# Performance work log

Hardware: AMD Instinct MI355X
Metric: run time of the kernel (lower is better)

## Reference

```python
import jax, jax.numpy as jnp
import numpy as np

D = 1024
H = 16
L = 2048
B = 2
EPS = 1e-5


def setup_inputs() -> dict:
    key = jax.random.key(0)
    ks = jax.random.split(key, 12)
    s = 0.02
    return {
        "x": jax.random.normal(ks[0], (B, L, D), dtype=jnp.float32),
        "ln1_w": jnp.ones((D,), jnp.float32),
        "ln1_b": jnp.zeros((D,), jnp.float32),
        "ln2_w": jnp.ones((D,), jnp.float32),
        "ln2_b": jnp.zeros((D,), jnp.float32),
        "attn_w": jax.random.normal(ks[1], (D, 3 * D), jnp.float32) * s,
        "attn_b": jnp.zeros((3 * D,), jnp.float32),
        "proj_w": jax.random.normal(ks[2], (D, D), jnp.float32) * s,
        "proj_b": jnp.zeros((D,), jnp.float32),
        "fc1_w": jax.random.normal(ks[3], (D, 4 * D), jnp.float32) * s,
        "fc1_b": jnp.zeros((4 * D,), jnp.float32),
        "fc2_w": jax.random.normal(ks[4], (4 * D, D), jnp.float32) * s,
        "fc2_b": jnp.zeros((D,), jnp.float32),
    }


def layernorm(x, w, b):
    mu = jnp.mean(x, axis=-1, keepdims=True)
    var = jnp.mean(jnp.square(x - mu), axis=-1, keepdims=True)
    return (x - mu) * jax.lax.rsqrt(var + EPS) * w + b


def reference(x, ln1_w, ln1_b, ln2_w, ln2_b, attn_w, attn_b,
              proj_w, proj_b, fc1_w, fc1_b, fc2_w, fc2_b):
    Bsz, Lq, C = x.shape
    hd = C // H

    # --- attention branch ---
    h = layernorm(x, ln1_w, ln1_b)
    qkv = h @ attn_w + attn_b                      # [B, L, 3C]
    q, k, v = jnp.split(qkv, 3, axis=-1)
    q = q.reshape(Bsz, Lq, H, hd).transpose(0, 2, 1, 3)  # [B, H, L, hd]
    k = k.reshape(Bsz, Lq, H, hd).transpose(0, 2, 1, 3)
    v = v.reshape(Bsz, Lq, H, hd).transpose(0, 2, 1, 3)

    # NOTE: original scales by 1/sqrt(embedding_dim), not sqrt(head_dim)
    att = jnp.einsum('bhqd,bhkd->bhqk', q, k) / jnp.sqrt(jnp.float32(C))
    causal = jnp.tril(jnp.ones((Lq, Lq), dtype=bool))
    att = jnp.where(causal[None, None], att, jnp.float32(-jnp.inf))
    att = jax.nn.softmax(att, axis=-1)
    y = jnp.einsum('bhqk,bhkd->bhqd', att, v)      # [B, H, L, hd]
    y = y.transpose(0, 2, 1, 3).reshape(Bsz, Lq, C)
    y = y @ proj_w + proj_b
    x = x + y

    # --- MLP branch ---
    h = layernorm(x, ln2_w, ln2_b)
    h = jax.nn.gelu(h @ fc1_w + fc1_b, approximate=False)
    h = h @ fc2_w + fc2_b
    return x + h
```

## Files before the change

### kernel.cpp

```cpp
#include <hip/hip_runtime.h>

#define Bsz 2
#define Lq  2048
#define Dm  1024
#define Hh  16

typedef __attribute__((ext_vector_type(8))) short bf16x8;
typedef __attribute__((ext_vector_type(4))) float f32x4;

#define MFMA16(a, b, c) __builtin_amdgcn_mfma_f32_16x16x32_bf16((a), (b), (c), 0, 0, 0)
#define EXP2F(x) __builtin_amdgcn_exp2f(x)

__device__ __forceinline__ short f2bf(float f) {
    union { float f; unsigned u; } v; v.f = f;
    unsigned r = v.u + 0x7fffu + ((v.u >> 16) & 1u);
    return (short)(r >> 16);
}

__device__ __forceinline__ float bf2f(unsigned short s) {
    union { float f; unsigned u; } t; t.u = ((unsigned)s) << 16;
    return t.f;
}

__device__ __forceinline__ int pk2(float a, float b) {
    union { float f; unsigned u; } ua, ub; ua.f = a; ub.f = b;
    return (int)((ua.u >> 16) | (ub.u & 0xffff0000u));
}

__device__ __forceinline__ void gload16(const void* g, void* l) {
    __builtin_amdgcn_global_load_lds((const __attribute__((address_space(1))) void*)g,
                                     (__attribute__((address_space(3))) void*)l,
                                     16, 0, 0);
}

__global__ __launch_bounds__(256) void ln_bf16(const float* __restrict__ x,
                                               const float* __restrict__ w,
                                               const float* __restrict__ b,
                                               short* __restrict__ out) {
    const int row = blockIdx.x;
    const int tid = threadIdx.x;
    const float4 v = ((const float4*)(x + (size_t)row * 1024))[tid];
    float s = v.x + v.y + v.z + v.w;
    float q = v.x * v.x + v.y * v.y + v.z * v.z + v.w * v.w;
    for (int off = 32; off > 0; off >>= 1) {
        s += __shfl_down(s, off);
        q += __shfl_down(q, off);
    }
    __shared__ float red[8];
    const int wave = tid >> 6;
    if ((tid & 63) == 0) { red[wave] = s; red[wave + 4] = q; }
    __syncthreads();
    s = red[0] + red[1] + red[2] + red[3];
    q = red[4] + red[5] + red[6] + red[7];
    const float mu = s * (1.0f / 1024.0f);
    const float var = q * (1.0f / 1024.0f) - mu * mu;
    const float rstd = rsqrtf(var + 1e-5f);
    const float4 wv = ((const float4*)w)[tid];
    const float4 bv = ((const float4*)b)[tid];
    short4 o;
    o.x = f2bf((v.x - mu) * rstd * wv.x + bv.x);
    o.y = f2bf((v.y - mu) * rstd * wv.y + bv.y);
    o.z = f2bf((v.z - mu) * rstd * wv.z + bv.z);
    o.w = f2bf((v.w - mu) * rstd * wv.w + bv.w);
    ((short4*)(out + (size_t)row * 1024))[tid] = o;
}

__global__ __launch_bounds__(256) void tr_cvt_all(
    const float* __restrict__ attnw, const float* __restrict__ projw,
    const float* __restrict__ fc1w,  const float* __restrict__ fc2w,
    short* __restrict__ attnwT, short* __restrict__ projwT,
    short* __restrict__ fc1wT,  short* __restrict__ fc2wT) {
    int id = blockIdx.x;
    const float* W; short* Wt; int K, N, bx, by;
    if (id < 3072)      { W = attnw; Wt = attnwT; K = 1024; N = 3072; bx = id % 96;  by = id / 96; }
    else if (id < 4096) { id -= 3072; W = projw; Wt = projwT; K = 1024; N = 1024; bx = id & 31; by = id >> 5; }
    else if (id < 8192) { id -= 4096; W = fc1w;  Wt = fc1wT;  K = 1024; N = 4096; bx = id & 127; by = id >> 7; }
    else                { id -= 8192; W = fc2w;  Wt = fc2wT;  K = 4096; N = 1024; bx = id & 31; by = id >> 5; }
    __shared__ float t[32][33];
    const int n0 = bx * 32, k0 = by * 32;
    const int tx = threadIdx.x & 31, ty = threadIdx.x >> 5;
#pragma unroll
    for (int i = 0; i < 4; i++)
        t[ty + i * 8][tx] = W[(size_t)(k0 + ty + i * 8) * N + n0 + tx];
    __syncthreads();
#pragma unroll
    for (int i = 0; i < 4; i++)
        Wt[(size_t)(n0 + ty + i * 8) * K + k0 + tx] = f2bf(t[tx][ty + i * 8]);
}

template <int EP>
__global__ __launch_bounds__(256, 4) void gemm_bt(
    const short* __restrict__ A, const short* __restrict__ Bt,
    const float* __restrict__ bias, int N, int K,
    short* __restrict__ qd, short* __restrict__ kd, short* __restrict__ vtd,
    short* __restrict__ outb) {
    __shared__ short As[128 * 64];
    __shared__ short Bs[128 * 64];
    const int tid = threadIdx.x;
    const int lane = tid & 63, w = tid >> 6;
    const int l16 = lane & 15, quad = lane >> 4;
    const int wr = (w & 1) * 64, wc = (w >> 1) * 64;
    const int n = blockIdx.x;
    const int row0 = ((n & 7) * 4 + ((n >> 3) & 3)) * 128;
    const int col0 = (n >> 5) * 128;
    const int srow = lane >> 3;
    const int scol = ((lane & 7) ^ srow) * 8;

    f32x4 acc[4][4];
    const f32x4 z = {0.f, 0.f, 0.f, 0.f};
#pragma unroll
    for (int i = 0; i < 4; i++)
#pragma unroll
        for (int j = 0; j < 4; j++) acc[i][j] = z;

    const size_t arow = (size_t)(row0 + w * 32 + srow);
    const size_t brow = (size_t)(col0 + w * 32 + srow);

    for (int k0 = 0; k0 < K; k0 += 64) {
#pragma unroll
        for (int g = 0; g < 4; g++) {
            gload16(A + (arow + g * 8) * K + k0 + scol,  &As[(w * 32 + g * 8) * 64]);
            gload16(Bt + (brow + g * 8) * K + k0 + scol, &Bs[(w * 32 + g * 8) * 64]);
        }
        __syncthreads();
#pragma unroll
        for (int kk = 0; kk < 2; kk++) {
            const int rsl = ((kk * 4 + quad) ^ (l16 & 7)) * 8;
            bf16x8 a[4], bb[4];
#pragma unroll
            for (int i = 0; i < 4; i++) a[i] = *(const bf16x8*)&As[(wr + i * 16 + l16) * 64 + rsl];
#pragma unroll
            for (int j = 0; j < 4; j++) bb[j] = *(const bf16x8*)&Bs[(wc + j * 16 + l16) * 64 + rsl];
#pragma unroll
            for (int i = 0; i < 4; i++)
#pragma unroll
                for (int j = 0; j < 4; j++) acc[i][j] = MFMA16(a[i], bb[j], acc[i][j]);
        }
        __syncthreads();
    }

    float bz[4];
#pragma unroll
    for (int j = 0; j < 4; j++) bz[j] = bias[col0 + wc + j * 16 + l16];

#pragma unroll
    for (int i = 0; i < 4; i++) {
#pragma unroll
        for (int r = 0; r < 4; r++) {
            const int grow = row0 + wr + i * 16 + quad * 4 + r;
#pragma unroll
            for (int j = 0; j < 4; j++) {
                const int gcol = col0 + wc + j * 16 + l16;
                const float v = acc[i][j][r] + bz[j];
                if constexpr (EP == 0) {
                    const int b = grow >> 11, l = grow & 2047;
                    const int sec = gcol >> 10, wi = gcol & 1023;
                    const int h = wi >> 6, d = wi & 63;
                    if (sec == 2) {
                        vtd[(((size_t)b * Hh + h) * 64 + d) * Lq + l] = f2bf(v);
                    } else {
                        short* dst = sec ? kd : qd;
                        dst[(((size_t)b * Hh + h) * Lq + l) * 64 + d] = f2bf(v);
                    }
                } else {
                    const float g = 0.5f * v * (1.0f + erff(v * 0.70710678118f));
                    outb[(size_t)grow * N + gcol] = f2bf(g);
                }
            }
        }
    }
}

__global__ __launch_bounds__(256, 4) void gemm_sk(
    const short* __restrict__ A, const short* __restrict__ Bt, int K, int zbits,
    short* __restrict__ Cp) {
    __shared__ short As[128 * 64];
    __shared__ short Bs[128 * 64];
    const int tid = threadIdx.x;
    const int lane = tid & 63, w = tid >> 6;
    const int l16 = lane & 15, quad = lane >> 4;
    const int wr = (w & 1) * 64, wc = (w >> 1) * 64;
    const int n = blockIdx.x;
    const int xcd = n & 7, t = n >> 3;
    const int col = t & 7, u = t >> 3;
    const int c = xcd * (4 << zbits) + u;
    const int zsl = c & ((1 << zbits) - 1);
    const int row0 = (c >> zbits) * 128, col0 = col * 128;
    const int KS = K >> zbits;
    const int kbeg = zsl * KS, kend = kbeg + KS;
    const int srow = lane >> 3;
    const int scol = ((lane & 7) ^ srow) * 8;

    f32x4 acc[4][4];
    const f32x4 z = {0.f, 0.f, 0.f, 0.f};
#pragma unroll
    for (int i = 0; i < 4; i++)
#pragma unroll
        for (int j = 0; j < 4; j++) acc[i][j] = z;

    const size_t arow = (size_t)(row0 + w * 32 + srow);
    const size_t brow = (size_t)(col0 + w * 32 + srow);

    for (int k0 = kbeg; k0 < kend; k0 += 64) {
#pragma unroll
        for (int g = 0; g < 4; g++) {
            gload16(A + (arow + g * 8) * K + k0 + scol,  &As[(w * 32 + g * 8) * 64]);
            gload16(Bt + (brow + g * 8) * K + k0 + scol, &Bs[(w * 32 + g * 8) * 64]);
        }
        __syncthreads();
#pragma unroll
        for (int kk = 0; kk < 2; kk++) {
            const int rsl = ((kk * 4 + quad) ^ (l16 & 7)) * 8;
            bf16x8 a[4], bb[4];
#pragma unroll
            for (int i = 0; i < 4; i++) a[i] = *(const bf16x8*)&As[(wr + i * 16 + l16) * 64 + rsl];
#pragma unroll
            for (int j = 0; j < 4; j++) bb[j] = *(const bf16x8*)&Bs[(wc + j * 16 + l16) * 64 + rsl];
#pragma unroll
            for (int i = 0; i < 4; i++)
#pragma unroll
                for (int j = 0; j < 4; j++) acc[i][j] = MFMA16(a[i], bb[j], acc[i][j]);
        }
        __syncthreads();
    }

    short* cp = Cp + (size_t)zsl * 4096 * 1024;
#pragma unroll
    for (int i = 0; i < 4; i++) {
#pragma unroll
        for (int r = 0; r < 4; r++) {
            const int grow = row0 + wr + i * 16 + quad * 4 + r;
#pragma unroll
            for (int j = 0; j < 4; j++) {
                const int gcol = col0 + wc + j * 16 + l16;
                cp[(size_t)grow * 1024 + gcol] = f2bf(acc[i][j][r]);
            }
        }
    }
}

__global__ __launch_bounds__(256) void sk_reduce(const short* __restrict__ Cp, int S,
                                                 const float* __restrict__ res,
                                                 const float* __restrict__ bias,
                                                 float* __restrict__ out) {
    const int row = blockIdx.x, tid = threadIdx.x;
    const size_t base = (size_t)row * 1024 + tid * 4;
    float4 a = ((const float4*)(res + (size_t)row * 1024))[tid];
    const float4 bz = ((const float4*)bias)[tid];
    a.x += bz.x; a.y += bz.y; a.z += bz.z; a.w += bz.w;
    for (int s = 0; s < S; s++) {
        const ushort4 c = *(const ushort4*)(Cp + (size_t)s * 4096 * 1024 + base);
        a.x += bf2f(c.x); a.y += bf2f(c.y); a.z += bf2f(c.z); a.w += bf2f(c.w);
    }
    *(float4*)(out + base) = a;
}

__global__ __launch_bounds__(256) void sk_reduce_ln(const short* __restrict__ Cp, int S,
                                                    const float* __restrict__ res,
                                                    const float* __restrict__ bias,
                                                    const float* __restrict__ lnw,
                                                    const float* __restrict__ lnb,
                                                    float* __restrict__ xout,
                                                    short* __restrict__ hout) {
    const int row = blockIdx.x, tid = threadIdx.x;
    const size_t base = (size_t)row * 1024 + tid * 4;
    float4 a = ((const float4*)(res + (size_t)row * 1024))[tid];
    const float4 bz = ((const float4*)bias)[tid];
    a.x += bz.x; a.y += bz.y; a.z += bz.z; a.w += bz.w;
    for (int s = 0; s < S; s++) {
        const ushort4 c = *(const ushort4*)(Cp + (size_t)s * 4096 * 1024 + base);
        a.x += bf2f(c.x); a.y += bf2f(c.y); a.z += bf2f(c.z); a.w += bf2f(c.w);
    }
    *(float4*)(xout + base) = a;
    float sm = a.x + a.y + a.z + a.w;
    float qs = a.x * a.x + a.y * a.y + a.z * a.z + a.w * a.w;
    for (int off = 32; off > 0; off >>= 1) {
        sm += __shfl_down(sm, off);
        qs += __shfl_down(qs, off);
    }
    __shared__ float red[8];
    const int wave = tid >> 6;
    if ((tid & 63) == 0) { red[wave] = sm; red[wave + 4] = qs; }
    __syncthreads();
    sm = red[0] + red[1] + red[2] + red[3];
    qs = red[4] + red[5] + red[6] + red[7];
    const float mu = sm * (1.0f / 1024.0f);
    const float var = qs * (1.0f / 1024.0f) - mu * mu;
    const float rstd = rsqrtf(var + 1e-5f);
    const float4 wv = ((const float4*)lnw)[tid];
    const float4 bv = ((const float4*)lnb)[tid];
    short4 o;
    o.x = f2bf((a.x - mu) * rstd * wv.x + bv.x);
    o.y = f2bf((a.y - mu) * rstd * wv.y + bv.y);
    o.z = f2bf((a.z - mu) * rstd * wv.z + bv.z);
    o.w = f2bf((a.w - mu) * rstd * wv.w + bv.w);
    ((short4*)(hout + (size_t)row * 1024))[tid] = o;
}

#define KP 72
__global__ __launch_bounds__(256, 2) void attn_kernel(const short* __restrict__ Q,
                                                      const short* __restrict__ Kb,
                                                      const short* __restrict__ Vt,
                                                      short* __restrict__ Y) {
    const int tid = threadIdx.x;
    const int lane = tid & 63, wave = tid >> 6;
    const int l16 = lane & 15, quad = lane >> 4;
    const int n = blockIdx.x;
    const int xcd = n & 7, m = n >> 3;
    const int bh = xcd * 4 + (m & 3);
    const int mm = (m & 31) >> 2;
    const int qblk = (m < 32) ? (15 - mm) : mm;
    const int qw = qblk * 128 + wave * 32;

    const short* qg = Q + ((size_t)bh * Lq + qw) * 64;
    const short* kg = Kb + (size_t)bh * Lq * 64;
    const short* vg = Vt + (size_t)bh * 64 * Lq;

    __shared__ short sK[2][64 * 64];
    __shared__ short sV[2][64 * 64];
    __shared__ short sP[4][32 * KP];
    short* wpP = sP[wave];

    const float c1 = 0.0450842213f;

    bf16x8 qf[2][2];
#pragma unroll
    for (int c = 0; c < 2; c++)
#pragma unroll
        for (int d = 0; d < 2; d++) {
            bf16x8 v = *(const bf16x8*)(qg + (c * 16 + l16) * 64 + d * 32 + quad * 8);
            bf16x8 r;
#pragma unroll
            for (int i = 0; i < 8; i++) {
                union { float f; unsigned u; } t;
                t.u = ((unsigned)(unsigned short)v[i]) << 16;
                r[i] = f2bf(t.f * c1);
            }
            qf[c][d] = r;
        }

    f32x4 o[4][2];
    const f32x4 z = {0.f, 0.f, 0.f, 0.f};
#pragma unroll
    for (int j = 0; j < 4; j++)
#pragma unroll
        for (int c = 0; c < 2; c++) o[j][c] = z;
    float l_i[2] = {0.f, 0.f};

    const int srow8 = lane >> 3;
    const int sslot = ((lane & 7) ^ srow8) * 8;
    const int r0 = wave * 16;
    const int nst = 2 * qblk + 2;

    auto stage = [&](int s) {
        const int p = s & 1;
        const int kb = s * 64;
        gload16(kg + (size_t)(kb + r0 + srow8) * 64 + sslot,     &sK[p][r0 * 64]);
        gload16(kg + (size_t)(kb + r0 + 8 + srow8) * 64 + sslot, &sK[p][(r0 + 8) * 64]);
        gload16(vg + (size_t)(r0 + srow8) * Lq + kb + sslot,     &sV[p][r0 * 64]);
        gload16(vg + (size_t)(r0 + 8 + srow8) * Lq + kb + sslot, &sV[p][(r0 + 8) * 64]);
    };

    stage(0);

    for (int s = 0; s < nst; ++s) {
        const int p = s & 1;
        __syncthreads();
        bf16x8 kf[4][2];
#pragma unroll
        for (int kt = 0; kt < 4; kt++)
#pragma unroll
            for (int d = 0; d < 2; d++)
                kf[kt][d] = *(const bf16x8*)&sK[p][(kt * 16 + l16) * 64 +
                                                   (((d * 4 + quad) ^ (l16 & 7)) * 8)];
        if (s + 1 < nst) stage(s + 1);

        f32x4 st[4][2];
#pragma unroll
        for (int kt = 0; kt < 4; kt++)
#pragma unroll
            for (int c = 0; c < 2; c++) {
                st[kt][c] = MFMA16(kf[kt][0], qf[c][0], z);
                st[kt][c] = MFMA16(kf[kt][1], qf[c][1], st[kt][c]);
            }

        const int rel = s * 64 - qblk * 128 - wave * 32;
        if (rel > -64) {
#pragma unroll
            for (int kt = 0; kt < 4; kt++)
#pragma unroll
                for (int c = 0; c < 2; c++)
#pragma unroll
                    for (int r = 0; r < 4; r++) {
                        const int krel = rel + kt * 16 + quad * 4 + r - c * 16;
                        if (krel > l16) st[kt][c][r] = -1e30f;
                    }
        }

#pragma unroll
        for (int c = 0; c < 2; c++) {
            float pv[4][4], rs = 0.f;
#pragma unroll
            for (int kt = 0; kt < 4; kt++)
#pragma unroll
                for (int r = 0; r < 4; r++) {
                    pv[kt][r] = EXP2F(st[kt][c][r]);
                    rs += pv[kt][r];
                }
            l_i[c] += rs;
            short* wp = wpP + (c * 16 + l16) * KP;
#pragma unroll
            for (int kt = 0; kt < 4; kt++) {
                int2 pw; pw.x = pk2(pv[kt][0], pv[kt][1]); pw.y = pk2(pv[kt][2], pv[kt][3]);
                *(int2*)(wp + kt * 16 + quad * 4) = pw;
            }
        }

        bf16x8 pf[2][2];
#pragma unroll
        for (int c = 0; c < 2; c++) {
            pf[c][0] = *(const bf16x8*)(wpP + (c * 16 + l16) * KP + quad * 8);
            pf[c][1] = *(const bf16x8*)(wpP + (c * 16 + l16) * KP + 32 + quad * 8);
        }
#pragma unroll
        for (int j = 0; j < 4; j++) {
            const bf16x8 v0 = *(const bf16x8*)&sV[p][(j * 16 + l16) * 64 +
                                                     ((quad ^ (l16 & 7)) * 8)];
            const bf16x8 v1 = *(const bf16x8*)&sV[p][(j * 16 + l16) * 64 +
                                                     (((4 + quad) ^ (l16 & 7)) * 8)];
#pragma unroll
            for (int c = 0; c < 2; c++) {
                o[j][c] = MFMA16(v0, pf[c][0], o[j][c]);
                o[j][c] = MFMA16(v1, pf[c][1], o[j][c]);
            }
        }
    }

    const int b = bh >> 4, h = bh & 15;
#pragma unroll
    for (int c = 0; c < 2; c++) {
        float ls = l_i[c];
        ls += __shfl_xor(ls, 16);
        ls += __shfl_xor(ls, 32);
        const float inv = 1.0f / ls;
        const size_t base = ((size_t)b * Lq + qw + c * 16 + l16) * 1024 + h * 64;
#pragma unroll
        for (int j = 0; j < 4; j++) {
            short4 s4;
            s4.x = f2bf(o[j][c][0] * inv);
            s4.y = f2bf(o[j][c][1] * inv);
            s4.z = f2bf(o[j][c][2] * inv);
            s4.w = f2bf(o[j][c][3] * inv);
            *(short4*)(Y + base + j * 16 + quad * 4) = s4;
        }
    }
}

extern "C" void kernel_launch(void* const* d_in, const int* in_sizes, int n_in,
                              void* d_out, int out_size, void* d_ws, size_t ws_size,
                              hipStream_t stream) {
    (void)in_sizes; (void)n_in; (void)out_size; (void)ws_size;
    const float* x     = (const float*)d_in[0];
    const float* ln1w  = (const float*)d_in[1];
    const float* ln1b  = (const float*)d_in[2];
    const float* ln2w  = (const float*)d_in[3];
    const float* ln2b  = (const float*)d_in[4];
    const float* attnw = (const float*)d_in[5];
    const float* attnb = (const float*)d_in[6];
    const float* projw = (const float*)d_in[7];
    const float* projb = (const float*)d_in[8];
    const float* fc1w  = (const float*)d_in[9];
    const float* fc1b  = (const float*)d_in[10];
    const float* fc2w  = (const float*)d_in[11];
    const float* fc2b  = (const float*)d_in[12];
    float* out = (float*)d_out;

    char* ws = (char*)d_ws;
    size_t off = 0;
    auto alloc = [&](size_t bytes) {
        void* p = ws + off;
        off += (bytes + 255) & ~(size_t)255;
        return p;
    };
    short* attnwT = (short*)alloc(3072ull * 1024 * 2);
    short* projwT = (short*)alloc(1024ull * 1024 * 2);
    short* fc1wT  = (short*)alloc(4096ull * 1024 * 2);
    short* fc2wT  = (short*)alloc(1024ull * 4096 * 2);
    short* hbuf   = (short*)alloc(4096ull * 1024 * 2);
    short* qbuf   = (short*)alloc(4096ull * 1024 * 2);
    short* kbuf   = (short*)alloc(4096ull * 1024 * 2);
    short* vtbuf  = (short*)alloc(4096ull * 1024 * 2);
    short* ybuf   = (short*)alloc(4096ull * 1024 * 2);
    float* x1     = (float*)alloc(4096ull * 1024 * 4);
    short* Cp     = (short*)alloc(4ull * 4096 * 1024 * 2);
    short* hh = qbuf;

    tr_cvt_all<<<12288, 256, 0, stream>>>(attnw, projw, fc1w, fc2w,
                                          attnwT, projwT, fc1wT, fc2wT);

    ln_bf16<<<4096, 256, 0, stream>>>(x, ln1w, ln1b, hbuf);
    gemm_bt<0><<<768, 256, 0, stream>>>(hbuf, attnwT, attnb, 3072, 1024,
                                        qbuf, kbuf, vtbuf, nullptr);
    attn_kernel<<<512, 256, 0, stream>>>(qbuf, kbuf, vtbuf, ybuf);
    gemm_sk<<<512, 256, 0, stream>>>(ybuf, projwT, 1024, 1, Cp);
    sk_reduce_ln<<<4096, 256, 0, stream>>>(Cp, 2, x, projb, ln2w, ln2b, x1, hbuf);

    gemm_bt<2><<<1024, 256, 0, stream>>>(hbuf, fc1wT, fc1b, 4096, 1024,
                                         nullptr, nullptr, nullptr, hh);
    gemm_sk<<<1024, 256, 0, stream>>>(hh, fc2wT, 4096, 2, Cp);
    sk_reduce<<<4096, 256, 0, stream>>>(Cp, 4, x1, fc2b, out);
}
```

Before: 325.3 us.

## Double-buffer LDS tiles in bf16 GEMM kernels to overlap loads with MFMA

Both GEMM kernels now use two LDS tile buffers and issue the next K-tile's global-to-LDS loads before computing on the current tile, with one barrier per tile instead of two. This aims to hide global memory latency behind MFMA work. It doubles LDS usage and lowers the launch-bounds occupancy hint from 4 to 2 blocks per CU. The loop assumes an even tile count.

```diff
diff --git a/kernel.cpp b/kernel.cpp
--- a/kernel.cpp
+++ b/kernel.cpp
@@ -89,13 +89,13 @@
 }
 
 template <int EP>
-__global__ __launch_bounds__(256, 4) void gemm_bt(
+__global__ __launch_bounds__(256, 2) void gemm_bt(
     const short* __restrict__ A, const short* __restrict__ Bt,
     const float* __restrict__ bias, int N, int K,
     short* __restrict__ qd, short* __restrict__ kd, short* __restrict__ vtd,
     short* __restrict__ outb) {
-    __shared__ short As[128 * 64];
-    __shared__ short Bs[128 * 64];
+    __shared__ short As0[128 * 64], Bs0[128 * 64];
+    __shared__ short As1[128 * 64], Bs1[128 * 64];
     const int tid = threadIdx.x;
     const int lane = tid & 63, w = tid >> 6;
     const int l16 = lane & 15, quad = lane >> 4;
@@ -116,27 +116,39 @@
     const size_t arow = (size_t)(row0 + w * 32 + srow);
     const size_t brow = (size_t)(col0 + w * 32 + srow);
 
-    for (int k0 = 0; k0 < K; k0 += 64) {
+    auto stage = [&](short* dA, short* dB, int t) {
+        const int k0 = t << 6;
 #pragma unroll
         for (int g = 0; g < 4; g++) {
-            gload16(A + (arow + g * 8) * K + k0 + scol,  &As[(w * 32 + g * 8) * 64]);
-            gload16(Bt + (brow + g * 8) * K + k0 + scol, &Bs[(w * 32 + g * 8) * 64]);
-        }
-        __syncthreads();
+            gload16(A + (arow + g * 8) * K + k0 + scol,  &dA[(w * 32 + g * 8) * 64]);
+            gload16(Bt + (brow + g * 8) * K + k0 + scol, &dB[(w * 32 + g * 8) * 64]);
+        }
+    };
+    auto compute = [&](const short* sA, const short* sB) {
 #pragma unroll
         for (int kk = 0; kk < 2; kk++) {
             const int rsl = ((kk * 4 + quad) ^ (l16 & 7)) * 8;
             bf16x8 a[4], bb[4];
 #pragma unroll
-            for (int i = 0; i < 4; i++) a[i] = *(const bf16x8*)&As[(wr + i * 16 + l16) * 64 + rsl];
-#pragma unroll
-            for (int j = 0; j < 4; j++) bb[j] = *(const bf16x8*)&Bs[(wc + j * 16 + l16) * 64 + rsl];
+            for (int i = 0; i < 4; i++) a[i] = *(const bf16x8*)&sA[(wr + i * 16 + l16) * 64 + rsl];
+#pragma unroll
+            for (int j = 0; j < 4; j++) bb[j] = *(const bf16x8*)&sB[(wc + j * 16 + l16) * 64 + rsl];
 #pragma unroll
             for (int i = 0; i < 4; i++)
 #pragma unroll
                 for (int j = 0; j < 4; j++) acc[i][j] = MFMA16(a[i], bb[j], acc[i][j]);
         }
+    };
+
+    const int NT = K >> 6;
+    stage(As0, Bs0, 0);
+    for (int t = 0; t < NT; t += 2) {
         __syncthreads();
+        if (t + 1 < NT) stage(As1, Bs1, t + 1);
+        compute(As0, Bs0);
+        __syncthreads();
+        if (t + 2 < NT) stage(As0, Bs0, t + 2);
+        compute(As1, Bs1);
     }
 
     float bz[4];
@@ -171,23 +183,23 @@
     }
 }
 
-__global__ __launch_bounds__(256, 4) void gemm_sk(
+__global__ __launch_bounds__(256, 2) void gemm_sk(
     const short* __restrict__ A, const short* __restrict__ Bt, int K, int zbits,
     short* __restrict__ Cp) {
-    __shared__ short As[128 * 64];
-    __shared__ short Bs[128 * 64];
+    __shared__ short As0[128 * 64], Bs0[128 * 64];
+    __shared__ short As1[128 * 64], Bs1[128 * 64];
     const int tid = threadIdx.x;
     const int lane = tid & 63, w = tid >> 6;
     const int l16 = lane & 15, quad = lane >> 4;
     const int wr = (w & 1) * 64, wc = (w >> 1) * 64;
     const int n = blockIdx.x;
-    const int xcd = n & 7, t = n >> 3;
-    const int col = t & 7, u = t >> 3;
+    const int xcd = n & 7, t0 = n >> 3;
+    const int col = t0 & 7, u = t0 >> 3;
     const int c = xcd * (4 << zbits) + u;
     const int zsl = c & ((1 << zbits) - 1);
     const int row0 = (c >> zbits) * 128, col0 = col * 128;
     const int KS = K >> zbits;
-    const int kbeg = zsl * KS, kend = kbeg + KS;
+    const int kbeg = zsl * KS;
     const int srow = lane >> 3;
     const int scol = ((lane & 7) ^ srow) * 8;
 
@@ -201,27 +213,39 @@
     const size_t arow = (size_t)(row0 + w * 32 + srow);
     const size_t brow = (size_t)(col0 + w * 32 + srow);
 
-    for (int k0 = kbeg; k0 < kend; k0 += 64) {
+    auto stage = [&](short* dA, short* dB, int t) {
+        const int k0 = kbeg + (t << 6);
 #pragma unroll
         for (int g = 0; g < 4; g++) {
-            gload16(A + (arow + g * 8) * K + k0 + scol,  &As[(w * 32 + g * 8) * 64]);
-            gload16(Bt + (brow + g * 8) * K + k0 + scol, &Bs[(w * 32 + g * 8) * 64]);
-        }
-        __syncthreads();
+            gload16(A + (arow + g * 8) * K + k0 + scol,  &dA[(w * 32 + g * 8) * 64]);
+            gload16(Bt + (brow + g * 8) * K + k0 + scol, &dB[(w * 32 + g * 8) * 64]);
+        }
+    };
+    auto compute = [&](const short* sA, const short* sB) {
 #pragma unroll
         for (int kk = 0; kk < 2; kk++) {
             const int rsl = ((kk * 4 + quad) ^ (l16 & 7)) * 8;
             bf16x8 a[4], bb[4];
 #pragma unroll
-            for (int i = 0; i < 4; i++) a[i] = *(const bf16x8*)&As[(wr + i * 16 + l16) * 64 + rsl];
-#pragma unroll
-            for (int j = 0; j < 4; j++) bb[j] = *(const bf16x8*)&Bs[(wc + j * 16 + l16) * 64 + rsl];
+            for (int i = 0; i < 4; i++) a[i] = *(const bf16x8*)&sA[(wr + i * 16 + l16) * 64 + rsl];
+#pragma unroll
+            for (int j = 0; j < 4; j++) bb[j] = *(const bf16x8*)&sB[(wc + j * 16 + l16) * 64 + rsl];
 #pragma unroll
             for (int i = 0; i < 4; i++)
 #pragma unroll
                 for (int j = 0; j < 4; j++) acc[i][j] = MFMA16(a[i], bb[j], acc[i][j]);
         }
+    };
+
+    const int NT = KS >> 6;
+    stage(As0, Bs0, 0);
+    for (int t = 0; t < NT; t += 2) {
         __syncthreads();
+        if (t + 1 < NT) stage(As1, Bs1, t + 1);
+        compute(As0, Bs0);
+        __syncthreads();
+        if (t + 2 < NT) stage(As0, Bs0, t + 2);
+        compute(As1, Bs1);
     }
 
     short* cp = Cp + (size_t)zsl * 4096 * 1024;
```

New measurement: 327.9 us. No clear change (+0.8%).
